# Optimization experiments

Measured on AMD Instinct MI355X. Metric: run time of the kernel, lower is better.

The kernel has to match this reference:

```python
import jax, jax.numpy as jnp
import numpy as np

N_EMBD = 2048
N_HEAD = 16
N_KV_HEAD = 4
HEAD_DIM = N_EMBD // N_HEAD
MAX_SEQ_LEN = 2048
EPS = 1e-6
ROPE_THETA = 10000.0


def _build_rope_cache(dim, max_seq_len, theta=ROPE_THETA):
    inv_freq = 1.0 / theta ** (np.arange(0, dim, 2, dtype=np.float32) / dim)
    t = np.arange(max_seq_len, dtype=np.float32)
    freqs = np.outer(t, inv_freq)
    emb = np.concatenate([freqs, freqs], axis=-1)
    return jnp.asarray(np.cos(emb)), jnp.asarray(np.sin(emb))


def _rotate_half(x):
    x1, x2 = jnp.split(x, 2, axis=-1)
    return jnp.concatenate([-x2, x1], axis=-1)


def _rms_norm(x, w, eps=EPS):
    var = jnp.mean(jnp.square(x), axis=-1, keepdims=True)
    return x * jax.lax.rsqrt(var + eps) * w


def setup_inputs() -> dict:
    key = jax.random.key(0)
    ks = jax.random.split(key, 7)
    s = 1.0 / np.sqrt(N_EMBD)
    kv_dim = N_KV_HEAD * HEAD_DIM
    x = jax.random.normal(ks[0], (2, 2048, N_EMBD), dtype=jnp.float32)
    Wq = jax.random.normal(ks[1], (N_EMBD, N_EMBD), dtype=jnp.float32) * s
    Wk = jax.random.normal(ks[2], (kv_dim, N_EMBD), dtype=jnp.float32) * s
    Wv = jax.random.normal(ks[3], (kv_dim, N_EMBD), dtype=jnp.float32) * s
    Wo = jax.random.normal(ks[4], (N_EMBD, N_EMBD), dtype=jnp.float32) * s
    qn_w = jnp.ones((HEAD_DIM,), dtype=jnp.float32)
    kn_w = jnp.ones((HEAD_DIM,), dtype=jnp.float32)
    cos, sin = _build_rope_cache(HEAD_DIM, MAX_SEQ_LEN)
    return {"x": x, "Wq": Wq, "Wk": Wk, "Wv": Wv, "Wo": Wo,
            "qn_w": qn_w, "kn_w": kn_w, "rope_cos": cos, "rope_sin": sin}


def reference(x, Wq, Wk, Wv, Wo, qn_w, kn_w, rope_cos, rope_sin):
    B, T, C = x.shape
    # projections (torch Linear: y = x @ W.T)
    q = jnp.einsum('btc,dc->btd', x, Wq).reshape(B, T, N_HEAD, HEAD_DIM).transpose(0, 2, 1, 3)
    k = jnp.einsum('btc,dc->btd', x, Wk).reshape(B, T, N_KV_HEAD, HEAD_DIM).transpose(0, 2, 1, 3)
    v = jnp.einsum('btc,dc->btd', x, Wv).reshape(B, T, N_KV_HEAD, HEAD_DIM).transpose(0, 2, 1, 3)
    # qk rms-norm
    q = _rms_norm(q, qn_w)
    k = _rms_norm(k, kn_w)
    # rope
    cos = rope_cos[:T][None, None]  # [1,1,T,D]
    sin = rope_sin[:T][None, None]
    q = q * cos + _rotate_half(q) * sin
    k = k * cos + _rotate_half(k) * sin
    # GQA broadcast: group queries over kv heads instead of repeating k/v
    G = N_HEAD // N_KV_HEAD
    qg = q.reshape(B, N_KV_HEAD, G, T, HEAD_DIM)
    scale = 1.0 / jnp.sqrt(jnp.asarray(HEAD_DIM, dtype=q.dtype))
    scores = jnp.einsum('bhgqd,bhkd->bhgqk', qg, k) * scale  # [B,KV,G,T,T]
    causal = jnp.tril(jnp.ones((T, T), dtype=bool))
    scores = jnp.where(causal, scores, jnp.asarray(-jnp.inf, dtype=scores.dtype))
    attn = jax.nn.softmax(scores, axis=-1)
    y = jnp.einsum('bhgqk,bhkd->bhgqd', attn, v)  # [B,KV,G,T,D]
    y = y.reshape(B, N_HEAD, T, HEAD_DIM).transpose(0, 2, 1, 3).reshape(B, T, C)
    return jnp.einsum('btc,dc->btd', y, Wo)
```

## Files before the change

kernel.cpp:

```cpp
#include <hip/hip_runtime.h>
#include <stdint.h>

typedef unsigned short u16;
typedef __attribute__((ext_vector_type(4))) float f32x4;
typedef __attribute__((ext_vector_type(16))) float f32x16;
typedef __attribute__((ext_vector_type(8))) short bf16x8;
typedef __attribute__((ext_vector_type(4))) unsigned short u16x4;
typedef __attribute__((ext_vector_type(4))) unsigned u32x4;

static __device__ __forceinline__ u16 f2bf(float f) {
  union { float f; unsigned u; } v; v.f = f;
  unsigned r = v.u + 0x7fffu + ((v.u >> 16) & 1u);
  return (u16)(r >> 16);
}
static __device__ __forceinline__ float bf2f(u16 u) {
  union { unsigned u; float f; } v; v.u = ((unsigned)u) << 16;
  return v.f;
}

static __device__ __forceinline__ unsigned cvtpk(float lo, float hi) {
  unsigned r;
  asm("v_cvt_pk_bf16_f32 %0, %1, %2" : "=v"(r) : "v"(lo), "v"(hi));
  return r;
}

static __device__ __forceinline__ void plane32_swap(unsigned& a, unsigned& b) {
  asm volatile("v_permlane32_swap_b32 %0, %1" : "+v"(a), "+v"(b));
}

static __device__ __forceinline__ float exp2_fast(float x) {
  float r;
  asm("v_exp_f32 %0, %1" : "=v"(r) : "v"(x));
  return r;
}

static __device__ __forceinline__ void load_lds16(const void* g, void* l) {
  __builtin_amdgcn_global_load_lds(
      (const __attribute__((address_space(1))) void*)g,
      (__attribute__((address_space(3))) void*)l, 16, 0, 0);
}


__global__ __launch_bounds__(256) void cvt_f32_bf16(
    const float* __restrict__ in, u16* __restrict__ out, int n) {
  int i = blockIdx.x * 256 + threadIdx.x;
  const int n4 = n >> 2;
  for (; i < n4; i += gridDim.x * 256) {
    f32x4 v = *(const f32x4*)(in + (size_t)i * 4);
    u16x4 o = { f2bf(v[0]), f2bf(v[1]), f2bf(v[2]), f2bf(v[3]) };
    *(u16x4*)(out + (size_t)i * 4) = o;
  }
}

__global__ __launch_bounds__(256) void build_wcat(
    const float* __restrict__ Wq, const float* __restrict__ Wk,
    const float* __restrict__ Wv, u16* __restrict__ out) {
  int i = blockIdx.x * 256 + threadIdx.x;
  const int n4 = 3072 * 512;
  for (; i < n4; i += gridDim.x * 256) {
    int row = i >> 9;
    int c4 = i & 511;
    const float* src;
    if (row < 2048)       src = Wq + (size_t)row * 2048;
    else if (row < 2560)  src = Wk + (size_t)(row - 2048) * 2048;
    else                  src = Wv + (size_t)(row - 2560) * 2048;
    f32x4 v = *(const f32x4*)(src + c4 * 4);
    u16x4 o = { f2bf(v[0]), f2bf(v[1]), f2bf(v[2]), f2bf(v[3]) };
    *(u16x4*)(out + (size_t)i * 4) = o;
  }
}

#define GEMM_CORE(C_STORE)                                                            \
  __shared__ u16 As[128 * 64];                                                        \
  __shared__ u16 Bs[128 * 64];                                                        \
  const int tid = threadIdx.x;                                                        \
  const int lin = blockIdx.x;                                                         \
  const int x = lin & 7, t = lin >> 3;                              \
  const int bm = x * 4 + (t & 3);                                                     \
  const int bn = t >> 2;                                                              \
  const int w = tid >> 6, l = tid & 63;                                               \
  const int wr = w >> 1, wc = w & 1;                                                  \
  const int ql = l & 31, hi = l >> 5;                                                 \
  f32x16 acc[2][2] = {};                                                              \
  const int nk = K >> 6;                                                              \
  for (int kt = 0; kt < nk; ++kt) {                                                   \
    __syncthreads();                                                                  \
    const int ko = kt << 6;                                                           \
    _Pragma("unroll")                                                                 \
    for (int j = 0; j < 4; ++j) {                                                     \
      int idx = j * 256 + tid;                                                        \
      int row = idx >> 3, ch = idx & 7;                                               \
      int col = ko + (((ch ^ (row & 7))) << 3);                                       \
      load_lds16(A + (size_t)(bm * 128 + row) * K + col, As + idx * 8);               \
      load_lds16(B + (size_t)(bn * 128 + row) * K + col, Bs + idx * 8);               \
    }                                                                                 \
    __syncthreads();                                                                  \
    _Pragma("unroll")                                                                 \
    for (int ks = 0; ks < 4; ++ks) {                                                  \
      const int e = ks * 2 + hi;                                                      \
      bf16x8 af[2], bfr[2];                                                           \
      _Pragma("unroll")                                                               \
      for (int ti = 0; ti < 2; ++ti) {                                                \
        const int ra = wr * 64 + ti * 32 + ql;                                        \
        const int rb = wc * 64 + ti * 32 + ql;                                        \
        af[ti]  = *(const bf16x8*)&As[ra * 64 + ((e ^ (ra & 7)) << 3)];               \
        bfr[ti] = *(const bf16x8*)&Bs[rb * 64 + ((e ^ (rb & 7)) << 3)];               \
      }                                                                               \
      _Pragma("unroll")                                                               \
      for (int mi = 0; mi < 2; ++mi)                                                  \
        _Pragma("unroll")                                                             \
        for (int ni = 0; ni < 2; ++ni)                                                \
          acc[mi][ni] = __builtin_amdgcn_mfma_f32_32x32x16_bf16(                      \
              af[mi], bfr[ni], acc[mi][ni], 0, 0, 0);                                 \
    }                                                                                 \
  }                                                                                   \
  _Pragma("unroll")                                                                   \
  for (int mi = 0; mi < 2; ++mi) {                                                    \
    const int rb0 = bm * 128 + wr * 64 + mi * 32;                                     \
    _Pragma("unroll")                                                                 \
    for (int ni = 0; ni < 2; ++ni) {                                                  \
      const int col = bn * 128 + wc * 64 + ni * 32 + ql;                              \
      _Pragma("unroll")                                                               \
      for (int r = 0; r < 16; ++r) {                                                  \
        const int row = rb0 + (r & 3) + 8 * (r >> 2) + 4 * hi;                        \
        C_STORE;                                                                      \
      }                                                                               \
    }                                                                                 \
  }

__global__ __launch_bounds__(256) void gemm_bt16(
    const u16* __restrict__ A, const u16* __restrict__ B,
    u16* __restrict__ C, int M, int N, int K) {
  GEMM_CORE(C[(size_t)row * N + col] = f2bf(acc[mi][ni][r]))
}

__global__ __launch_bounds__(256) void gemm_bt(
    const u16* __restrict__ A, const u16* __restrict__ B,
    float* __restrict__ C, int M, int N, int K) {
  GEMM_CORE(C[(size_t)row * N + col] = acc[mi][ni][r])
}

__global__ __launch_bounds__(256) void norm_rope(
    const u16* __restrict__ qkv, const float* __restrict__ qn_w,
    const float* __restrict__ kn_w, const float* __restrict__ cosb,
    const float* __restrict__ sinb, u16* __restrict__ qhat,
    u16* __restrict__ khat) {
  const int gw = (blockIdx.x * 256 + threadIdx.x) >> 6;
  const int lane = threadIdx.x & 63;
  const int slot = gw % 20;
  const int row = gw / 20;
  const int t = row & 2047;
  const int b = row >> 11;
  const u16* src; const float* nw; u16* dst;
  bool isq = slot < 16;
  if (isq) {
    src = qkv + (size_t)row * 3072 + slot * 128;
    nw = qn_w;
    dst = qhat + ((size_t)(b * 16 + slot) * 2048 + t) * 128;
  } else {
    src = qkv + (size_t)row * 3072 + 2048 + (slot - 16) * 128;
    nw = kn_w;
    dst = khat + ((size_t)(b * 4 + (slot - 16)) * 2048 + t) * 128;
  }
  float x1 = bf2f(src[lane]), x2 = bf2f(src[lane + 64]);
  float ss = x1 * x1 + x2 * x2;
#pragma unroll
  for (int o = 32; o; o >>= 1) ss += __shfl_xor(ss, o);
  float rs = rsqrtf(ss * (1.0f / 128.0f) + 1e-6f);
  float h1 = x1 * rs * nw[lane];
  float h2 = x2 * rs * nw[lane + 64];
  float c = cosb[t * 128 + lane], s = sinb[t * 128 + lane];
  float o1 = h1 * c - h2 * s;
  float o2 = h2 * c + h1 * s;
  if (isq) { o1 *= 0.12751744752f; o2 *= 0.12751744752f; }
  dst[lane] = f2bf(o1);
  dst[lane + 64] = f2bf(o2);
}

__global__ __launch_bounds__(256) void v_trans(
    const u16* __restrict__ qkv, u16* __restrict__ vT) {
  __shared__ u16 st[64][130];
  const int bi = blockIdx.x;
  const int tt = bi & 31;
  const int kv = (bi >> 5) & 3;
  const int b = bi >> 7;
  const int tid = threadIdx.x;
#pragma unroll
  for (int i = 0; i < 32; ++i) {
    int idx = i * 256 + tid;
    int t = idx >> 7, d = idx & 127;
    st[t][d] = qkv[(size_t)(b * 2048 + tt * 64 + t) * 3072 + 2560 + kv * 128 + d];
  }
  __syncthreads();
#pragma unroll
  for (int i = 0; i < 32; ++i) {
    int idx = i * 256 + tid;
    int d = idx >> 6, t = idx & 63;
    vT[((size_t)(b * 4 + kv) * 128 + d) * 2048 + tt * 64 + t] = st[t][d];
  }
}

__global__ __launch_bounds__(256, 2) void attn(
    const u16* __restrict__ qhat, const u16* __restrict__ khat,
    const u16* __restrict__ vT, u16* __restrict__ yb) {
  __shared__ u16 Kt[2][64 * 128];
  __shared__ u16 Vt[2][128 * 64];
  const int bi = blockIdx.x;
  const int j = bi & 255;
  const int pairup = bi >> 8;
  const int bh = j >> 3;
  const int cc = j & 7;
  const int c = pairup ? (15 - cc) : cc;
  const int h = bh & 15, b = bh >> 4;
  const int kvh = h >> 2;
  const int tid = threadIdx.x;
  const int w = tid >> 6, l = tid & 63;
  const int ql = l & 31, hi = l >> 5;
  const int wq0 = c * 128 + w * 32;
  const int wq_end = wq0 + 31;
  const int qg = wq0 + ql;

  bf16x8 qf[8];
  const u16* qp = qhat + ((size_t)(b * 16 + h) * 2048 + qg) * 128 + hi * 8;
#pragma unroll
  for (int sf = 0; sf < 8; ++sf) qf[sf] = *(const bf16x8*)(qp + 16 * sf);

  f32x16 yacc[4] = {};
  float m = -1e30f, lsum = 0.f;

  const u16* Kg = khat + (size_t)(b * 4 + kvh) * 2048 * 128;
  const u16* Vg = vT + (size_t)(b * 4 + kvh) * 128 * 2048;
  const int nt = 2 * c + 2;

  auto stageK = [&](int tile, int buf) {
#pragma unroll
    for (int jj = 0; jj < 4; ++jj) {
      int idx = jj * 256 + tid;
      int row = idx >> 4, ch = idx & 15;
      load_lds16(Kg + (size_t)(tile * 64 + row) * 128 + ((ch ^ (row & 7)) * 8),
                 &Kt[buf][idx * 8]);
    }
  };
  auto stageV = [&](int tile, int buf) {
#pragma unroll
    for (int jj = 0; jj < 4; ++jj) {
      int idx = jj * 256 + tid;
      int row = idx >> 3, ch = idx & 7;
      load_lds16(Vg + (size_t)row * 2048 + tile * 64 + ((ch ^ (row & 7)) * 8),
                 &Vt[buf][idx * 8]);
    }
  };

  stageK(0, 0);
  stageV(0, 0);
  int cur = 0;
  for (int tile = 0; tile < nt; ++tile) {
    const int kv0 = tile * 64;
    __syncthreads();
    if (tile + 1 < nt) { stageK(tile + 1, cur ^ 1); stageV(tile + 1, cur ^ 1); }
    if (kv0 <= wq_end) {
      const u16* Kc = Kt[cur];
      const u16* Vc = Vt[cur];
      f32x16 sacc[2] = {};
      __builtin_amdgcn_s_setprio(1);
#pragma unroll
      for (int n = 0; n < 2; ++n) {
#pragma unroll
        for (int sf = 0; sf < 8; ++sf) {
          bf16x8 kf = *(const bf16x8*)&Kc[(n * 32 + ql) * 128 + (((2 * sf + hi) ^ (l & 7)) * 8)];
          sacc[n] = __builtin_amdgcn_mfma_f32_32x32x16_bf16(kf, qf[sf], sacc[n], 0, 0, 0);
        }
      }
      __builtin_amdgcn_s_setprio(0);
      if (kv0 + 63 > wq0) {
#pragma unroll
        for (int n = 0; n < 2; ++n)
#pragma unroll
          for (int r = 0; r < 16; ++r) {
            int kv = kv0 + n * 32 + (r & 3) + 8 * (r >> 2) + 4 * hi;
            if (kv > qg) sacc[n][r] = -1e30f;
          }
      }
      float pm = -1e30f;
#pragma unroll
      for (int n = 0; n < 2; ++n)
#pragma unroll
        for (int r = 0; r < 16; ++r) pm = fmaxf(pm, sacc[n][r]);
      pm = fmaxf(pm, __shfl_xor(pm, 32));
      if (!__all(pm - m <= 11.0f)) {
        float mn = fmaxf(m, pm);
        float sc = exp2_fast(m - mn);
        m = mn;
        lsum *= sc;
#pragma unroll
        for (int r = 0; r < 16; ++r) {
          int row = (r & 3) + 8 * (r >> 2) + 4 * hi;
          float scr = __shfl(sc, row);
#pragma unroll
          for (int d = 0; d < 4; ++d) yacc[d][r] *= scr;
        }
      }
      float ls = 0.f;
#pragma unroll
      for (int n = 0; n < 2; ++n)
#pragma unroll
        for (int r = 0; r < 16; ++r) {
          float e = exp2_fast(sacc[n][r] - m);
          sacc[n][r] = e;
          ls += e;
        }
      ls += __shfl_xor(ls, 32);
      lsum += ls;
      bf16x8 pa[4];
#pragma unroll
      for (int s4 = 0; s4 < 4; ++s4) {
        const int n = s4 >> 1, R = (s4 & 1) * 8;
        unsigned P01 = cvtpk(sacc[n][R + 0], sacc[n][R + 1]);
        unsigned P23 = cvtpk(sacc[n][R + 2], sacc[n][R + 3]);
        unsigned P45 = cvtpk(sacc[n][R + 4], sacc[n][R + 5]);
        unsigned P67 = cvtpk(sacc[n][R + 6], sacc[n][R + 7]);
        plane32_swap(P01, P45);
        plane32_swap(P23, P67);
        union { u32x4 u; bf16x8 bv; } cvu;
        cvu.u[0] = P01; cvu.u[1] = P23; cvu.u[2] = P45; cvu.u[3] = P67;
        pa[s4] = cvu.bv;
      }
      __builtin_amdgcn_s_setprio(1);
#pragma unroll
      for (int d = 0; d < 4; ++d) {
        const int rv = d * 32 + ql;
#pragma unroll
        for (int ks = 0; ks < 4; ++ks) {
          bf16x8 vf = *(const bf16x8*)&Vc[rv * 64 + (((ks * 2 + hi) ^ (rv & 7)) * 8)];
          yacc[d] = __builtin_amdgcn_mfma_f32_32x32x16_bf16(pa[ks], vf, yacc[d], 0, 0, 0);
        }
      }
      __builtin_amdgcn_s_setprio(0);
    }
    cur ^= 1;
  }
#pragma unroll
  for (int r = 0; r < 16; ++r) {
    int row = (r & 3) + 8 * (r >> 2) + 4 * hi;
    float li = __shfl(lsum, row);
    float inv = 1.0f / li;
    u16* yp = yb + ((size_t)(b * 2048) + wq0 + row) * 2048 + h * 128 + ql;
#pragma unroll
    for (int d = 0; d < 4; ++d) yp[d * 32] = f2bf(yacc[d][r] * inv);
  }
}


extern "C" void kernel_launch(void* const* d_in, const int* in_sizes, int n_in,
                              void* d_out, int out_size, void* d_ws, size_t ws_size,
                              hipStream_t stream) {
  const float* x    = (const float*)d_in[0];
  const float* Wq   = (const float*)d_in[1];
  const float* Wk   = (const float*)d_in[2];
  const float* Wv   = (const float*)d_in[3];
  const float* Wo   = (const float*)d_in[4];
  const float* qn   = (const float*)d_in[5];
  const float* kn   = (const float*)d_in[6];
  const float* cosb = (const float*)d_in[7];
  const float* sinb = (const float*)d_in[8];
  float* out = (float*)d_out;
  (void)in_sizes; (void)n_in; (void)out_size; (void)ws_size;

  char* p = (char*)d_ws;
  u16*   xb   = (u16*)p;   p += (size_t)8388608 * 2;
  u16*   wcat = (u16*)p;   p += (size_t)6291456 * 2;
  u16*   wob  = (u16*)p;   p += (size_t)4194304 * 2;
  u16*   qkvb = (u16*)p;   p += (size_t)12582912 * 2;
  u16*   qh   = (u16*)p;   p += (size_t)8388608 * 2;
  u16*   kh   = (u16*)p;   p += (size_t)2097152 * 2;
  u16*   vt   = (u16*)p;   p += (size_t)2097152 * 2;
  u16*   yb   = (u16*)p;   p += (size_t)8388608 * 2;

  cvt_f32_bf16<<<2048, 256, 0, stream>>>(x, xb, 8388608);
  build_wcat<<<2048, 256, 0, stream>>>(Wq, Wk, Wv, wcat);
  cvt_f32_bf16<<<2048, 256, 0, stream>>>(Wo, wob, 4194304);
  gemm_bt16<<<768, 256, 0, stream>>>(xb, wcat, qkvb, 4096, 3072, 2048);
  norm_rope<<<20480, 256, 0, stream>>>(qkvb, qn, kn, cosb, sinb, qh, kh);
  v_trans<<<256, 256, 0, stream>>>(qkvb, vt);
  attn<<<512, 256, 0, stream>>>(qh, kh, vt, yb);
  gemm_bt<<<512, 256, 0, stream>>>(yb, wob, out, 4096, 2048, 2048);
}
```

Measured before the change: 212.0 us.

## Shrink attention blocks to two waves with 32-key tiles and single-buffered V

The attention kernel now uses 128-thread blocks covering 64 queries, launched on 1024 blocks. Each loop step walks 32 keys instead of 64, and V is single-buffered with a new rotation swizzle. V is loaded in the same iteration it is consumed, with an added barrier before the PV MFMAs. The intent is to cut LDS use per block and improve occupancy and load balance across CUs. In exchange, V load latency is no longer hidden by prefetch, and each key tile pays two barriers for half the MFMA work.

```diff
diff --git a/kernel.cpp b/kernel.cpp
--- a/kernel.cpp
+++ b/kernel.cpp
@@ -200,23 +200,22 @@
   }
 }
 
-__global__ __launch_bounds__(256, 2) void attn(
+__global__ __launch_bounds__(128) void attn(
     const u16* __restrict__ qhat, const u16* __restrict__ khat,
     const u16* __restrict__ vT, u16* __restrict__ yb) {
-  __shared__ u16 Kt[2][64 * 128];
-  __shared__ u16 Vt[2][128 * 64];
+  __shared__ u16 Kt[2][32 * 128];
+  __shared__ u16 Vt[128 * 32];
   const int bi = blockIdx.x;
-  const int j = bi & 255;
-  const int pairup = bi >> 8;
-  const int bh = j >> 3;
-  const int cc = j & 7;
-  const int c = pairup ? (15 - cc) : cc;
+  const int j = bi & 511;
+  const int bh = j >> 4;
+  const int cc = j & 15;
+  const int c = (bi < 512) ? cc : (31 - cc);
   const int h = bh & 15, b = bh >> 4;
   const int kvh = h >> 2;
   const int tid = threadIdx.x;
   const int w = tid >> 6, l = tid & 63;
   const int ql = l & 31, hi = l >> 5;
-  const int wq0 = c * 128 + w * 32;
+  const int wq0 = c * 64 + w * 32;
   const int wq_end = wq0 + 31;
   const int qg = wq0 + ql;
 
@@ -235,57 +234,51 @@
   auto stageK = [&](int tile, int buf) {
 #pragma unroll
     for (int jj = 0; jj < 4; ++jj) {
-      int idx = jj * 256 + tid;
+      int idx = jj * 128 + tid;
       int row = idx >> 4, ch = idx & 15;
-      load_lds16(Kg + (size_t)(tile * 64 + row) * 128 + ((ch ^ (row & 7)) * 8),
+      load_lds16(Kg + (size_t)(tile * 32 + row) * 128 + ((ch ^ (row & 7)) * 8),
                  &Kt[buf][idx * 8]);
     }
   };
-  auto stageV = [&](int tile, int buf) {
+  auto stageV = [&](int tile) {
 #pragma unroll
     for (int jj = 0; jj < 4; ++jj) {
-      int idx = jj * 256 + tid;
-      int row = idx >> 3, ch = idx & 7;
-      load_lds16(Vg + (size_t)row * 2048 + tile * 64 + ((ch ^ (row & 7)) * 8),
-                 &Vt[buf][idx * 8]);
+      int idx = jj * 128 + tid;
+      int d = idx >> 2, ck = idx & 3;
+      int e = (ck - (d >> 1)) & 3;
+      load_lds16(Vg + (size_t)d * 2048 + tile * 32 + e * 8, &Vt[idx * 8]);
     }
   };
 
   stageK(0, 0);
-  stageV(0, 0);
   int cur = 0;
   for (int tile = 0; tile < nt; ++tile) {
-    const int kv0 = tile * 64;
+    const int kv0 = tile * 32;
     __syncthreads();
-    if (tile + 1 < nt) { stageK(tile + 1, cur ^ 1); stageV(tile + 1, cur ^ 1); }
-    if (kv0 <= wq_end) {
+    if (tile + 1 < nt) stageK(tile + 1, cur ^ 1);
+    stageV(tile);
+    const bool act = (kv0 <= wq_end);
+    bf16x8 pa[2];
+    if (act) {
       const u16* Kc = Kt[cur];
-      const u16* Vc = Vt[cur];
-      f32x16 sacc[2] = {};
+      f32x16 sacc = {};
       __builtin_amdgcn_s_setprio(1);
 #pragma unroll
-      for (int n = 0; n < 2; ++n) {
-#pragma unroll
-        for (int sf = 0; sf < 8; ++sf) {
-          bf16x8 kf = *(const bf16x8*)&Kc[(n * 32 + ql) * 128 + (((2 * sf + hi) ^ (l & 7)) * 8)];
-          sacc[n] = __builtin_amdgcn_mfma_f32_32x32x16_bf16(kf, qf[sf], sacc[n], 0, 0, 0);
+      for (int sf = 0; sf < 8; ++sf) {
+        bf16x8 kf = *(const bf16x8*)&Kc[ql * 128 + (((2 * sf + hi) ^ (ql & 7)) * 8)];
+        sacc = __builtin_amdgcn_mfma_f32_32x32x16_bf16(kf, qf[sf], sacc, 0, 0, 0);
+      }
+      __builtin_amdgcn_s_setprio(0);
+      if (kv0 + 31 > wq0) {
+#pragma unroll
+        for (int r = 0; r < 16; ++r) {
+          int kv = kv0 + (r & 3) + 8 * (r >> 2) + 4 * hi;
+          if (kv > qg) sacc[r] = -1e30f;
         }
       }
-      __builtin_amdgcn_s_setprio(0);
-      if (kv0 + 63 > wq0) {
-#pragma unroll
-        for (int n = 0; n < 2; ++n)
-#pragma unroll
-          for (int r = 0; r < 16; ++r) {
-            int kv = kv0 + n * 32 + (r & 3) + 8 * (r >> 2) + 4 * hi;
-            if (kv > qg) sacc[n][r] = -1e30f;
-          }
-      }
       float pm = -1e30f;
 #pragma unroll
-      for (int n = 0; n < 2; ++n)
-#pragma unroll
-        for (int r = 0; r < 16; ++r) pm = fmaxf(pm, sacc[n][r]);
+      for (int r = 0; r < 16; ++r) pm = fmaxf(pm, sacc[r]);
       pm = fmaxf(pm, __shfl_xor(pm, 32));
       if (!__all(pm - m <= 11.0f)) {
         float mn = fmaxf(m, pm);
@@ -302,36 +295,37 @@
       }
       float ls = 0.f;
 #pragma unroll
-      for (int n = 0; n < 2; ++n)
-#pragma unroll
-        for (int r = 0; r < 16; ++r) {
-          float e = exp2_fast(sacc[n][r] - m);
-          sacc[n][r] = e;
-          ls += e;
-        }
+      for (int r = 0; r < 16; ++r) {
+        float e = exp2_fast(sacc[r] - m);
+        sacc[r] = e;
+        ls += e;
+      }
       ls += __shfl_xor(ls, 32);
       lsum += ls;
-      bf16x8 pa[4];
-#pragma unroll
-      for (int s4 = 0; s4 < 4; ++s4) {
-        const int n = s4 >> 1, R = (s4 & 1) * 8;
-        unsigned P01 = cvtpk(sacc[n][R + 0], sacc[n][R + 1]);
-        unsigned P23 = cvtpk(sacc[n][R + 2], sacc[n][R + 3]);
-        unsigned P45 = cvtpk(sacc[n][R + 4], sacc[n][R + 5]);
-        unsigned P67 = cvtpk(sacc[n][R + 6], sacc[n][R + 7]);
+#pragma unroll
+      for (int s2 = 0; s2 < 2; ++s2) {
+        const int R = s2 * 8;
+        unsigned P01 = cvtpk(sacc[R + 0], sacc[R + 1]);
+        unsigned P23 = cvtpk(sacc[R + 2], sacc[R + 3]);
+        unsigned P45 = cvtpk(sacc[R + 4], sacc[R + 5]);
+        unsigned P67 = cvtpk(sacc[R + 6], sacc[R + 7]);
         plane32_swap(P01, P45);
         plane32_swap(P23, P67);
         union { u32x4 u; bf16x8 bv; } cvu;
         cvu.u[0] = P01; cvu.u[1] = P23; cvu.u[2] = P45; cvu.u[3] = P67;
-        pa[s4] = cvu.bv;
-      }
+        pa[s2] = cvu.bv;
+      }
+    }
+    __syncthreads();
+    if (act) {
       __builtin_amdgcn_s_setprio(1);
 #pragma unroll
       for (int d = 0; d < 4; ++d) {
         const int rv = d * 32 + ql;
 #pragma unroll
-        for (int ks = 0; ks < 4; ++ks) {
-          bf16x8 vf = *(const bf16x8*)&Vc[rv * 64 + (((ks * 2 + hi) ^ (rv & 7)) * 8)];
+        for (int ks = 0; ks < 2; ++ks) {
+          const int e = ks * 2 + hi;
+          bf16x8 vf = *(const bf16x8*)&Vt[rv * 32 + (((e + (rv >> 1)) & 3) * 8)];
           yacc[d] = __builtin_amdgcn_mfma_f32_32x32x16_bf16(pa[ks], vf, yacc[d], 0, 0, 0);
         }
       }
@@ -382,6 +376,6 @@
   gemm_bt16<<<768, 256, 0, stream>>>(xb, wcat, qkvb, 4096, 3072, 2048);
   norm_rope<<<20480, 256, 0, stream>>>(qkvb, qn, kn, cosb, sinb, qh, kh);
   v_trans<<<256, 256, 0, stream>>>(qkvb, vt);
-  attn<<<512, 256, 0, stream>>>(qh, kh, vt, yb);
+  attn<<<1024, 128, 0, stream>>>(qh, kh, vt, yb);
   gemm_bt<<<512, 256, 0, stream>>>(yb, wob, out, 4096, 2048, 2048);
 }
```

Result: slower. 253.1 us (+19.4%).
